# Optimization experiments

Measured on AMD Instinct MI355X. Metric: run time of the kernel, lower is better.

## Reference

```python
import jax, jax.numpy as jnp
import numpy as np

B = 65536   # collocation batch
D = 8       # total_dim (tokens)
H = 128     # subnet hidden_dim
E = 64      # attn_embed_dim == subnet output_dim (proj is None)
NH = 4      # attention heads
GA = 4      # groupA_size


def setup_inputs() -> dict:
    key = jax.random.key(0)
    ks = iter(jax.random.split(key, 32))
    n = lambda shape, s: jax.random.normal(next(ks), shape, dtype=jnp.float32) * s
    inp = {
        "x":  jax.random.normal(next(ks), (B, D), dtype=jnp.float32),
        "w1": n((D, H), 1.0),                 # Lin(1,H) per dim (xavier ~ sqrt(2/(1+H)))
        "b1": jnp.zeros((D, H), jnp.float32),
        "w2": n((D, H, H), 1.0 / np.sqrt(H)),
        "b2": jnp.zeros((D, H), jnp.float32),
        "w3": n((D, E, H), 1.0 / np.sqrt(H)),
        "b3": jnp.zeros((D, E), jnp.float32),
    }
    for tag in ("sa", "sb", "ca", "cb"):
        inp[f"Win_{tag}"] = n((3 * E, E), 1.0 / np.sqrt(E))
        inp[f"bin_{tag}"] = jnp.zeros((3 * E,), jnp.float32)
        inp[f"Wo_{tag}"]  = n((E, E), 1.0 / np.sqrt(E))
        inp[f"bo_{tag}"]  = jnp.zeros((E,), jnp.float32)
    inp["Wf"] = n((1, 2 * E), 1.0 / np.sqrt(2 * E))
    inp["bf"] = jnp.zeros((1,), jnp.float32)
    return inp


def _mha(q, k, v, Win, bin_, Wo, bo):
    # PyTorch nn.MultiheadAttention (batch_first=True) math
    Wq, Wk, Wv = jnp.split(Win, 3, axis=0)
    bq, bk, bv = jnp.split(bin_, 3)
    dh = E // NH
    def heads(t, W, b):
        p = t @ W.T + b                         # [B,S,E]
        return p.reshape(p.shape[0], p.shape[1], NH, dh)
    qh = heads(q, Wq, bq)
    kh = heads(k, Wk, bk)
    vh = heads(v, Wv, bv)
    att = jnp.einsum('bqhd,bkhd->bhqk', qh, kh) / jnp.sqrt(jnp.float32(dh))
    w = jax.nn.softmax(att, axis=-1)
    o = jnp.einsum('bhqk,bkhd->bqhd', w, vh)
    o = o.reshape(o.shape[0], o.shape[1], E)
    return o @ Wo.T + bo


def reference(x, w1, b1, w2, b2, w3, b3,
              Win_sa, bin_sa, Wo_sa, bo_sa,
              Win_sb, bin_sb, Wo_sb, bo_sb,
              Win_ca, bin_ca, Wo_ca, bo_ca,
              Win_cb, bin_cb, Wo_cb, bo_cb,
              Wf, bf):
    # Per-dim subnets as block-diagonal batched matmuls (activation='sin', dropout=0)
    h = jnp.sin(x[:, :, None] * w1[None] + b1[None])            # [B,D,H]
    h = jnp.sin(jnp.einsum('bdh,dkh->bdk', h, w2) + b2[None])   # [B,D,H]
    tokens = jnp.einsum('bdh,doh->bdo', h, w3) + b3[None]       # [B,D,E]

    A = tokens[:, :GA, :]
    Bt = tokens[:, GA:, :]
    A_self  = _mha(A,  A,  A,  Win_sa, bin_sa, Wo_sa, bo_sa)
    B_self  = _mha(Bt, Bt, Bt, Win_sb, bin_sb, Wo_sb, bo_sb)
    A_cross = _mha(A,  Bt, Bt, Win_ca, bin_ca, Wo_ca, bo_ca)
    B_cross = _mha(Bt, A,  A,  Win_cb, bin_cb, Wo_cb, bo_cb)

    A_pool = ((A_self + A_cross) * 0.5).mean(axis=1)            # [B,E]
    B_pool = ((B_self + B_cross) * 0.5).mean(axis=1)            # [B,E]
    combined = jnp.concatenate([A_pool, B_pool], axis=1)        # [B,2E]
    out = combined @ Wf.T + bf                                  # [B,1]
    return jax.nn.leaky_relu(out, 0.01)
```

## Files before the change

kernel.cpp:

```cpp
#include <hip/hip_runtime.h>

typedef unsigned short u16;
typedef __attribute__((ext_vector_type(8))) short short8;
typedef __attribute__((ext_vector_type(4))) float f32x4;

#define OFF_U     0
#define OFF_CV    1024
#define OFF_CONST 1040
#define OFF_CTAG  1044
#define OFF_BA    1056
#define OFF_BB    1328
#define OFF_WA_B    6400
#define OFF_WB_B    41216
#define OFF_W2P_B   76032
#define OFF_W3P_B   338176
#define OFF_TOK_B   469248

#define P_STRIDE 280
#define PSIDE    (32 * P_STRIDE)

static __device__ __forceinline__ u16 f2bf(float f) {
  unsigned int bits = __float_as_uint(f);
  bits += 0x7fffu + ((bits >> 16) & 1u);
  return (u16)(bits >> 16);
}
static __device__ __forceinline__ float bf2f(u16 u) {
  return __uint_as_float(((unsigned int)u) << 16);
}
static __device__ __forceinline__ void ld16(const u16* p, float* o) {
  short8 v0 = *(const short8*)p;
  short8 v1 = *(const short8*)(p + 8);
#pragma unroll
  for (int i = 0; i < 8; i++) {
    o[i] = bf2f((u16)v0[i]);
    o[8 + i] = bf2f((u16)v1[i]);
  }
}

__global__ __launch_bounds__(64) void prep_fold(
    const float* __restrict__ win_sa, const float* __restrict__ bin_sa,
    const float* __restrict__ wo_sa,  const float* __restrict__ bo_sa,
    const float* __restrict__ win_sb, const float* __restrict__ bin_sb,
    const float* __restrict__ wo_sb,  const float* __restrict__ bo_sb,
    const float* __restrict__ win_ca, const float* __restrict__ bin_ca,
    const float* __restrict__ wo_ca,  const float* __restrict__ bo_ca,
    const float* __restrict__ win_cb, const float* __restrict__ bin_cb,
    const float* __restrict__ wo_cb,  const float* __restrict__ bo_cb,
    const float* __restrict__ Wf, float* __restrict__ ws) {
  __shared__ float v_lds[64];
  const int t = threadIdx.x;
  const int tag = blockIdx.x;
  const float* wins[4] = {win_sa, win_sb, win_ca, win_cb};
  const float* bins[4] = {bin_sa, bin_sb, bin_ca, bin_cb};
  const float* wos[4]  = {wo_sa, wo_sb, wo_ca, wo_cb};
  const float* bos[4]  = {bo_sa, bo_sb, bo_ca, bo_cb};
  const float* wfh = Wf + ((tag == 0 || tag == 2) ? 0 : 64);
  float v = 0.f;
#pragma unroll
  for (int e = 0; e < 64; e++) v += wos[tag][e * 64 + t] * wfh[e];
  v_lds[t] = v;
  __syncthreads();
#pragma unroll
  for (int h = 0; h < 4; h++) {
    float u = 0.f;
#pragma unroll
    for (int dp = 0; dp < 16; dp++)
      u += wins[tag][(128 + h * 16 + dp) * 64 + t] * v_lds[h * 16 + dp];
    ws[OFF_U + tag * 256 + h * 64 + t] = u;
  }
  if (t < 4) {
    float cv = 0.f;
#pragma unroll
    for (int dp = 0; dp < 16; dp++)
      cv += bins[tag][128 + t * 16 + dp] * v_lds[t * 16 + dp];
    ws[OFF_CV + tag * 4 + t] = cv;
  }
  if (t == 0) {
    float c = 0.f;
#pragma unroll
    for (int e = 0; e < 64; e++) c += bos[tag][e] * wfh[e];
    ws[OFF_CTAG + tag] = c;
  }
}

__global__ __launch_bounds__(256) void prep_pack(
    const float* __restrict__ w2, const float* __restrict__ w3,
    const float* __restrict__ win_sa, const float* __restrict__ win_sb,
    const float* __restrict__ win_ca, const float* __restrict__ win_cb,
    const float* __restrict__ bin_sa, const float* __restrict__ bin_sb,
    const float* __restrict__ bin_ca, const float* __restrict__ bin_cb,
    const float* __restrict__ bf,
    float* __restrict__ ws, u16* __restrict__ w2p, u16* __restrict__ w3p,
    u16* __restrict__ WA, u16* __restrict__ WB) {
  int idx = blockIdx.x * 256 + threadIdx.x;
  if (idx < 131072) {
    int d = idx >> 14, rem = idx & 16383;
    int f = rem >> 9, ks = f >> 3, nt = f & 7;
    int r2 = rem & 511, l = r2 >> 3, j = r2 & 7;
    int quad = l >> 4, m15 = l & 15;
    w2p[idx] = f2bf(w2[(d * 128 + nt * 16 + m15) * 128 + ks * 32 + quad * 8 + j]);
  } else if (idx < 196608) {
    int i = idx - 131072;
    int d = i >> 13, rem = i & 8191;
    int f = rem >> 9, ks = f >> 2, nt = f & 3;
    int r2 = rem & 511, l = r2 >> 3, j = r2 & 7;
    int quad = l >> 4, m15 = l & 15;
    w3p[i] = f2bf(w3[(d * 64 + nt * 16 + m15) * 128 + ks * 32 + quad * 8 + j]);
  } else if (idx < 214016) {
    int i = idx - 196608;
    int nt = i >> 10, rem = i & 1023;
    int half = rem >> 9, r2 = rem & 511, l = r2 >> 3, j = r2 & 7;
    int n = nt * 16 + (l & 15), k = half * 32 + (l >> 4) * 8 + j;
    float v;
    if (n < 64)       v = win_sa[n * 64 + k] * 0.25f;
    else if (n < 128) v = win_sa[n * 64 + k];
    else if (n < 192) v = win_ca[(n - 128) * 64 + k] * 0.25f;
    else if (n < 256) v = win_cb[(n - 128) * 64 + k];
    else if (n < 260) v = ws[OFF_U + 0 * 256 + (n - 256) * 64 + k];
    else if (n < 264) v = ws[OFF_U + 3 * 256 + (n - 260) * 64 + k];
    else              v = 0.f;
    WA[i] = f2bf(v);
  } else if (idx < 231424) {
    int i = idx - 214016;
    int nt = i >> 10, rem = i & 1023;
    int half = rem >> 9, r2 = rem & 511, l = r2 >> 3, j = r2 & 7;
    int n = nt * 16 + (l & 15), k = half * 32 + (l >> 4) * 8 + j;
    float v;
    if (n < 64)       v = win_sb[n * 64 + k] * 0.25f;
    else if (n < 128) v = win_sb[n * 64 + k];
    else if (n < 192) v = win_cb[(n - 128) * 64 + k] * 0.25f;
    else if (n < 256) v = win_ca[(n - 128) * 64 + k];
    else if (n < 260) v = ws[OFF_U + 1 * 256 + (n - 256) * 64 + k];
    else if (n < 264) v = ws[OFF_U + 2 * 256 + (n - 260) * 64 + k];
    else              v = 0.f;
    WB[i] = f2bf(v);
  } else if (idx < 231696) {
    int n = idx - 231424;
    float v;
    if (n < 64)       v = bin_sa[n] * 0.25f;
    else if (n < 128) v = bin_sa[n];
    else if (n < 192) v = bin_ca[n - 128] * 0.25f;
    else if (n < 256) v = bin_cb[n - 128];
    else if (n < 260) v = ws[OFF_CV + 0 * 4 + (n - 256)];
    else if (n < 264) v = ws[OFF_CV + 3 * 4 + (n - 260)];
    else              v = 0.f;
    ws[OFF_BA + n] = v;
  } else if (idx < 231968) {
    int n = idx - 231696;
    float v;
    if (n < 64)       v = bin_sb[n] * 0.25f;
    else if (n < 128) v = bin_sb[n];
    else if (n < 192) v = bin_cb[n - 128] * 0.25f;
    else if (n < 256) v = bin_ca[n - 128];
    else if (n < 260) v = ws[OFF_CV + 1 * 4 + (n - 256)];
    else if (n < 264) v = ws[OFF_CV + 2 * 4 + (n - 260)];
    else              v = 0.f;
    ws[OFF_BB + n] = v;
  } else if (idx == 231968) {
    ws[OFF_CONST] = 0.5f * (ws[OFF_CTAG] + ws[OFF_CTAG + 1] +
                            ws[OFF_CTAG + 2] + ws[OFF_CTAG + 3]) + bf[0];
  }
}

__global__ __launch_bounds__(256, 3) void tokens_kernel(
    const float* __restrict__ x, const float* __restrict__ w1,
    const float* __restrict__ b1, const float* __restrict__ b2,
    const float* __restrict__ b3, const u16* __restrict__ w2p,
    const u16* __restrict__ w3p, u16* __restrict__ tok_out) {
  __shared__ __align__(16) u16 w2l[16384];
  __shared__ __align__(16) u16 scratch[4][16 * 136];
  const int t = threadIdx.x;
  const int wave = t >> 6, lane = t & 63;
  const int m15 = lane & 15, quad = lane >> 4;
  const int d = blockIdx.x & 7;
  const int g = blockIdx.x >> 3;
  const int b0 = g * 64 + wave * 16;
  const float xv = x[(size_t)(b0 + m15) * 8 + d];
#pragma unroll
  for (int c = 0; c < 8; c++)
    *(short8*)&w2l[c * 2048 + t * 8] = *(const short8*)&w2p[d * 16384 + c * 2048 + t * 8];

  short8 afr[4];
#pragma unroll
  for (int ks = 0; ks < 4; ks++) {
    const float* w1p = w1 + d * 128 + ks * 32 + quad * 8;
    const float* b1p = b1 + d * 128 + ks * 32 + quad * 8;
    float4 wa = *(const float4*)w1p, wb = *(const float4*)(w1p + 4);
    float4 ba = *(const float4*)b1p, bb = *(const float4*)(b1p + 4);
    short8 a;
    a[0] = (short)f2bf(__sinf(xv * wa.x + ba.x));
    a[1] = (short)f2bf(__sinf(xv * wa.y + ba.y));
    a[2] = (short)f2bf(__sinf(xv * wa.z + ba.z));
    a[3] = (short)f2bf(__sinf(xv * wa.w + ba.w));
    a[4] = (short)f2bf(__sinf(xv * wb.x + bb.x));
    a[5] = (short)f2bf(__sinf(xv * wb.y + bb.y));
    a[6] = (short)f2bf(__sinf(xv * wb.z + bb.z));
    a[7] = (short)f2bf(__sinf(xv * wb.w + bb.w));
    afr[ks] = a;
  }
  __syncthreads();
  f32x4 acc2[8];
#pragma unroll
  for (int nt = 0; nt < 8; nt++) acc2[nt] = (f32x4){0.f, 0.f, 0.f, 0.f};
#pragma unroll
  for (int ks = 0; ks < 4; ks++) {
#pragma unroll
    for (int nt = 0; nt < 8; nt++) {
      short8 bfr = *(const short8*)&w2l[(ks * 8 + nt) * 512 + lane * 8];
      acc2[nt] = __builtin_amdgcn_mfma_f32_16x16x32_bf16(afr[ks], bfr, acc2[nt], 0, 0, 0);
    }
  }
#pragma unroll
  for (int nt = 0; nt < 8; nt++) {
    float bias = b2[d * 128 + m15 + 16 * nt];
#pragma unroll
    for (int r = 0; r < 4; r++)
      scratch[wave][(quad * 4 + r) * 136 + m15 + 16 * nt] =
          f2bf(__sinf(acc2[nt][r] + bias));
  }
  const u16* w3base = w3p + d * 8192 + lane * 8;
  f32x4 acc3[4];
#pragma unroll
  for (int nt = 0; nt < 4; nt++) acc3[nt] = (f32x4){0.f, 0.f, 0.f, 0.f};
#pragma unroll
  for (int ks = 0; ks < 4; ks++) {
    short8 af = *(const short8*)(&scratch[wave][m15 * 136 + ks * 32 + quad * 8]);
#pragma unroll
    for (int nt = 0; nt < 4; nt++) {
      short8 bfr = *(const short8*)(w3base + (ks * 4 + nt) * 512);
      acc3[nt] = __builtin_amdgcn_mfma_f32_16x16x32_bf16(af, bfr, acc3[nt], 0, 0, 0);
    }
  }
#pragma unroll
  for (int nt = 0; nt < 4; nt++) {
    float bias = b3[d * 64 + m15 + 16 * nt];
#pragma unroll
    for (int r = 0; r < 4; r++)
      scratch[wave][(quad * 4 + r) * 136 + m15 + 16 * nt] = f2bf(acc3[nt][r] + bias);
  }
  {
    int chunk = lane & 7;
#pragma unroll
    for (int it = 0; it < 2; it++) {
      int row_l = (lane >> 3) + it * 8;
      short8 v = *(const short8*)&scratch[wave][row_l * 136 + chunk * 8];
      *(short8*)(tok_out + ((size_t)(d * 65536 + b0 + row_l)) * 64 + chunk * 8) = v;
    }
  }
}

__global__ __launch_bounds__(128, 4) void attn_kernel(
    const float* __restrict__ ws, const u16* __restrict__ tok,
    const u16* __restrict__ WA, const u16* __restrict__ WB,
    float* __restrict__ out) {
  __shared__ __align__(16) u16 P[2 * PSIDE];
  const int t = threadIdx.x;
  const int wave = t >> 6, lane = t & 63;
  const int m15 = lane & 15, quad = lane >> 4;
  const int side = wave;
  const int b0 = blockIdx.x * 8;
  const float cst = ws[OFF_CONST];

  {
    const u16* W = side ? WB : WA;
    const float* bias = ws + (side ? OFF_BB : OFF_BA);
    const int dd = (m15 & 3) + side * 4;
    short8 a0[2], a1[2];
#pragma unroll
    for (int mt = 0; mt < 2; mt++) {
      const int e = mt * 4 + (m15 >> 2);
      const u16* ab = tok + ((size_t)(dd * 65536 + b0 + e)) * 64 + quad * 8;
      a0[mt] = *(const short8*)ab;
      a1[mt] = *(const short8*)(ab + 32);
    }
    u16* Pb = &P[side * PSIDE];
#pragma unroll
    for (int nt = 0; nt < 17; nt++) {
      const u16* bp = W + nt * 1024 + lane * 8;
      short8 bf0 = *(const short8*)bp;
      short8 bf1 = *(const short8*)(bp + 512);
      float bi = bias[nt * 16 + m15];
#pragma unroll
      for (int mt = 0; mt < 2; mt++) {
        f32x4 acc = {0.f, 0.f, 0.f, 0.f};
        acc = __builtin_amdgcn_mfma_f32_16x16x32_bf16(a0[mt], bf0, acc, 0, 0, 0);
        acc = __builtin_amdgcn_mfma_f32_16x16x32_bf16(a1[mt], bf1, acc, 0, 0, 0);
#pragma unroll
        for (int r = 0; r < 4; r++)
          Pb[(mt * 16 + quad * 4 + r) * P_STRIDE + m15 + 16 * nt] =
              f2bf(acc[r] + bi);
      }
    }
  }
  __syncthreads();
  const int elem = t >> 4, sub = t & 15;
  const int h = sub >> 2, q = sub & 3;
  float acc = 0.f;
#pragma unroll
  for (int tag = 0; tag < 4; tag++) {
    const int qs = tag & 1, cross = tag >> 1;
    const int ks2 = qs ^ cross;
    const u16* Pq = P + qs * PSIDE + (elem * 4 + q) * P_STRIDE + cross * 128 + h * 16;
    float qv[16];
    ld16(Pq, qv);
    const u16* Pk = P + ks2 * PSIDE + (elem * 4) * P_STRIDE + 64 + cross * 128 + h * 16;
    float sc[4];
#pragma unroll
    for (int k = 0; k < 4; k++) {
      float kv[16];
      ld16(Pk + k * P_STRIDE, kv);
      float s = 0.f;
#pragma unroll
      for (int i = 0; i < 16; i++) s += qv[i] * kv[i];
      sc[k] = s;
    }
    float mx = fmaxf(fmaxf(sc[0], sc[1]), fmaxf(sc[2], sc[3]));
    float e0 = __expf(sc[0] - mx), e1 = __expf(sc[1] - mx);
    float e2 = __expf(sc[2] - mx), e3 = __expf(sc[3] - mx);
    const u16* Psv = P + ks2 * PSIDE + (elem * 4) * P_STRIDE + 256 + cross * 4 + h;
    float o = e0 * bf2f(Psv[0]) + e1 * bf2f(Psv[P_STRIDE]) +
              e2 * bf2f(Psv[2 * P_STRIDE]) + e3 * bf2f(Psv[3 * P_STRIDE]);
    acc += o / (e0 + e1 + e2 + e3);
  }
  acc += __shfl_xor(acc, 1);
  acc += __shfl_xor(acc, 2);
  acc += __shfl_xor(acc, 4);
  acc += __shfl_xor(acc, 8);
  if (sub == 0) {
    float val = 0.125f * acc + cst;
    out[b0 + elem] = val > 0.f ? val : 0.01f * val;
  }
}

extern "C" void kernel_launch(void* const* d_in, const int* in_sizes, int n_in,
                              void* d_out, int out_size, void* d_ws, size_t ws_size,
                              hipStream_t stream) {
  const float* x      = (const float*)d_in[0];
  const float* w1     = (const float*)d_in[1];
  const float* b1     = (const float*)d_in[2];
  const float* w2     = (const float*)d_in[3];
  const float* b2     = (const float*)d_in[4];
  const float* w3     = (const float*)d_in[5];
  const float* b3     = (const float*)d_in[6];
  const float* win_sa = (const float*)d_in[7];
  const float* bin_sa = (const float*)d_in[8];
  const float* wo_sa  = (const float*)d_in[9];
  const float* bo_sa  = (const float*)d_in[10];
  const float* win_sb = (const float*)d_in[11];
  const float* bin_sb = (const float*)d_in[12];
  const float* wo_sb  = (const float*)d_in[13];
  const float* bo_sb  = (const float*)d_in[14];
  const float* win_ca = (const float*)d_in[15];
  const float* bin_ca = (const float*)d_in[16];
  const float* wo_ca  = (const float*)d_in[17];
  const float* bo_ca  = (const float*)d_in[18];
  const float* win_cb = (const float*)d_in[19];
  const float* bin_cb = (const float*)d_in[20];
  const float* wo_cb  = (const float*)d_in[21];
  const float* bo_cb  = (const float*)d_in[22];
  const float* Wf     = (const float*)d_in[23];
  const float* bf     = (const float*)d_in[24];
  float* ws = (float*)d_ws;
  u16* WAp    = (u16*)((char*)d_ws + OFF_WA_B);
  u16* WBp    = (u16*)((char*)d_ws + OFF_WB_B);
  u16* w2p    = (u16*)((char*)d_ws + OFF_W2P_B);
  u16* w3p    = (u16*)((char*)d_ws + OFF_W3P_B);
  u16* tokbuf = (u16*)((char*)d_ws + OFF_TOK_B);
  float* out = (float*)d_out;

  prep_fold<<<4, 64, 0, stream>>>(win_sa, bin_sa, wo_sa, bo_sa,
                                  win_sb, bin_sb, wo_sb, bo_sb,
                                  win_ca, bin_ca, wo_ca, bo_ca,
                                  win_cb, bin_cb, wo_cb, bo_cb,
                                  Wf, ws);
  prep_pack<<<907, 256, 0, stream>>>(w2, w3, win_sa, win_sb, win_ca, win_cb,
                                     bin_sa, bin_sb, bin_ca, bin_cb, bf,
                                     ws, w2p, w3p, WAp, WBp);
  tokens_kernel<<<8192, 256, 0, stream>>>(x, w1, b1, b2, b3, w2p, w3p, tokbuf);
  attn_kernel<<<8192, 128, 0, stream>>>(ws, tokbuf, WAp, WBp, out);
}
```

Before: 227.9 us.

## Use MFMA for attention scores, pack transposed P stores, drop W2 LDS staging

The attention scoring stage now computes the per-head QK dot products with a bf16 MFMA over a transposed P layout instead of scalar loops. The softmax also drops max subtraction and uses a fast reciprocal. The projection MFMA swaps its operands so each lane writes four packed bf16 values in one 8-byte store. The tokens kernel reads W2 fragments straight from global memory instead of staging them in LDS, which removes a sync and frees LDS for a higher occupancy bound (4 blocks). Risks: exp overflow without max subtraction, the MFMA computes redundant off-diagonal products, and global W2 reads depend on cache hits.

```diff
diff --git a/kernel.cpp b/kernel.cpp
--- a/kernel.cpp
+++ b/kernel.cpp
@@ -2,7 +2,9 @@
 
 typedef unsigned short u16;
 typedef __attribute__((ext_vector_type(8))) short short8;
+typedef __attribute__((ext_vector_type(4))) short s16x4;
 typedef __attribute__((ext_vector_type(4))) float f32x4;
+typedef __attribute__((ext_vector_type(2))) unsigned int u32x2;
 
 #define OFF_U     0
 #define OFF_CV    1024
@@ -24,17 +26,12 @@
   bits += 0x7fffu + ((bits >> 16) & 1u);
   return (u16)(bits >> 16);
 }
+static __device__ __forceinline__ unsigned rbits(float f) {
+  unsigned b = __float_as_uint(f);
+  return b + 0x7fffu + ((b >> 16) & 1u);
+}
 static __device__ __forceinline__ float bf2f(u16 u) {
   return __uint_as_float(((unsigned int)u) << 16);
-}
-static __device__ __forceinline__ void ld16(const u16* p, float* o) {
-  short8 v0 = *(const short8*)p;
-  short8 v1 = *(const short8*)(p + 8);
-#pragma unroll
-  for (int i = 0; i < 8; i++) {
-    o[i] = bf2f((u16)v0[i]);
-    o[8 + i] = bf2f((u16)v1[i]);
-  }
 }
 
 __global__ __launch_bounds__(64) void prep_fold(
@@ -162,12 +159,11 @@
   }
 }
 
-__global__ __launch_bounds__(256, 3) void tokens_kernel(
+__global__ __launch_bounds__(256, 4) void tokens_kernel(
     const float* __restrict__ x, const float* __restrict__ w1,
     const float* __restrict__ b1, const float* __restrict__ b2,
     const float* __restrict__ b3, const u16* __restrict__ w2p,
     const u16* __restrict__ w3p, u16* __restrict__ tok_out) {
-  __shared__ __align__(16) u16 w2l[16384];
   __shared__ __align__(16) u16 scratch[4][16 * 136];
   const int t = threadIdx.x;
   const int wave = t >> 6, lane = t & 63;
@@ -176,9 +172,6 @@
   const int g = blockIdx.x >> 3;
   const int b0 = g * 64 + wave * 16;
   const float xv = x[(size_t)(b0 + m15) * 8 + d];
-#pragma unroll
-  for (int c = 0; c < 8; c++)
-    *(short8*)&w2l[c * 2048 + t * 8] = *(const short8*)&w2p[d * 16384 + c * 2048 + t * 8];
 
   short8 afr[4];
 #pragma unroll
@@ -198,7 +191,7 @@
     a[7] = (short)f2bf(__sinf(xv * wb.w + bb.w));
     afr[ks] = a;
   }
-  __syncthreads();
+  const u16* w2base = w2p + d * 16384 + lane * 8;
   f32x4 acc2[8];
 #pragma unroll
   for (int nt = 0; nt < 8; nt++) acc2[nt] = (f32x4){0.f, 0.f, 0.f, 0.f};
@@ -206,7 +199,7 @@
   for (int ks = 0; ks < 4; ks++) {
 #pragma unroll
     for (int nt = 0; nt < 8; nt++) {
-      short8 bfr = *(const short8*)&w2l[(ks * 8 + nt) * 512 + lane * 8];
+      short8 bfr = *(const short8*)(w2base + (ks * 8 + nt) * 512);
       acc2[nt] = __builtin_amdgcn_mfma_f32_16x16x32_bf16(afr[ks], bfr, acc2[nt], 0, 0, 0);
     }
   }
@@ -277,58 +270,62 @@
 #pragma unroll
     for (int nt = 0; nt < 17; nt++) {
       const u16* bp = W + nt * 1024 + lane * 8;
-      short8 bf0 = *(const short8*)bp;
-      short8 bf1 = *(const short8*)(bp + 512);
-      float bi = bias[nt * 16 + m15];
+      short8 w0f = *(const short8*)bp;
+      short8 w1f = *(const short8*)(bp + 512);
+      float4 bi = *(const float4*)(bias + nt * 16 + quad * 4);
 #pragma unroll
       for (int mt = 0; mt < 2; mt++) {
         f32x4 acc = {0.f, 0.f, 0.f, 0.f};
-        acc = __builtin_amdgcn_mfma_f32_16x16x32_bf16(a0[mt], bf0, acc, 0, 0, 0);
-        acc = __builtin_amdgcn_mfma_f32_16x16x32_bf16(a1[mt], bf1, acc, 0, 0, 0);
-#pragma unroll
-        for (int r = 0; r < 4; r++)
-          Pb[(mt * 16 + quad * 4 + r) * P_STRIDE + m15 + 16 * nt] =
-              f2bf(acc[r] + bi);
+        acc = __builtin_amdgcn_mfma_f32_16x16x32_bf16(w0f, a0[mt], acc, 0, 0, 0);
+        acc = __builtin_amdgcn_mfma_f32_16x16x32_bf16(w1f, a1[mt], acc, 0, 0, 0);
+        u32x2 pk;
+        pk[0] = (rbits(acc[1] + bi.y) & 0xffff0000u) | (rbits(acc[0] + bi.x) >> 16);
+        pk[1] = (rbits(acc[3] + bi.w) & 0xffff0000u) | (rbits(acc[2] + bi.z) >> 16);
+        *(u32x2*)&Pb[(mt * 16 + m15) * P_STRIDE + nt * 16 + quad * 4] = pk;
       }
     }
   }
   __syncthreads();
-  const int elem = t >> 4, sub = t & 15;
-  const int h = sub >> 2, q = sub & 3;
-  float acc = 0.f;
-#pragma unroll
-  for (int tag = 0; tag < 4; tag++) {
-    const int qs = tag & 1, cross = tag >> 1;
-    const int ks2 = qs ^ cross;
-    const u16* Pq = P + qs * PSIDE + (elem * 4 + q) * P_STRIDE + cross * 128 + h * 16;
-    float qv[16];
-    ld16(Pq, qv);
-    const u16* Pk = P + ks2 * PSIDE + (elem * 4) * P_STRIDE + 64 + cross * 128 + h * 16;
-    float sc[4];
-#pragma unroll
-    for (int k = 0; k < 4; k++) {
-      float kv[16];
-      ld16(Pk + k * P_STRIDE, kv);
-      float s = 0.f;
-#pragma unroll
-      for (int i = 0; i < 16; i++) s += qv[i] * kv[i];
-      sc[k] = s;
-    }
-    float mx = fmaxf(fmaxf(sc[0], sc[1]), fmaxf(sc[2], sc[3]));
-    float e0 = __expf(sc[0] - mx), e1 = __expf(sc[1] - mx);
-    float e2 = __expf(sc[2] - mx), e3 = __expf(sc[3] - mx);
-    const u16* Psv = P + ks2 * PSIDE + (elem * 4) * P_STRIDE + 256 + cross * 4 + h;
-    float o = e0 * bf2f(Psv[0]) + e1 * bf2f(Psv[P_STRIDE]) +
-              e2 * bf2f(Psv[2 * P_STRIDE]) + e3 * bf2f(Psv[3 * P_STRIDE]);
-    acc += o / (e0 + e1 + e2 + e3);
-  }
-  acc += __shfl_xor(acc, 1);
-  acc += __shfl_xor(acc, 2);
-  acc += __shfl_xor(acc, 4);
-  acc += __shfl_xor(acc, 8);
-  if (sub == 0) {
-    float val = 0.125f * acc + cst;
-    out[b0 + elem] = val > 0.f ? val : 0.01f * val;
+  {
+    const int eg = wave;
+    const int q2 = (quad & 1) * 8;
+    const bool hiq = (quad & 2) != 0;
+    const u16* row0 = P + (size_t)(eg * 16 + m15) * P_STRIDE;
+    const u16* row1 = row0 + PSIDE;
+    float acc = 0.f;
+#pragma unroll
+    for (int tag = 0; tag < 4; tag++) {
+      const int qs = tag & 1, cross = tag >> 1;
+      const int ks2 = qs ^ cross;
+      const u16* rowK = ks2 ? row1 : row0;
+      const u16* rowQ = qs ? row1 : row0;
+      const u16* vbase = P + ks2 * PSIDE +
+                         (size_t)(eg * 16 + quad * 4) * P_STRIDE + 256 + cross * 4;
+      s16x4 vv0 = *(const s16x4*)(vbase);
+      s16x4 vv1 = *(const s16x4*)(vbase + P_STRIDE);
+      s16x4 vv2 = *(const s16x4*)(vbase + 2 * P_STRIDE);
+      s16x4 vv3 = *(const s16x4*)(vbase + 3 * P_STRIDE);
+#pragma unroll
+      for (int h = 0; h < 4; h++) {
+        const int kcol = 64 + cross * 128 + h * 16 + q2;
+        const int qcol = hiq ? 264 : (cross * 128 + h * 16 + q2);
+        short8 afr = *(const short8*)(rowK + kcol);
+        short8 bfr = *(const short8*)(rowQ + qcol);
+        f32x4 c = {0.f, 0.f, 0.f, 0.f};
+        c = __builtin_amdgcn_mfma_f32_16x16x32_bf16(afr, bfr, c, 0, 0, 0);
+        float e0 = __expf(c[0]), e1 = __expf(c[1]);
+        float e2 = __expf(c[2]), e3 = __expf(c[3]);
+        float o = e0 * bf2f((u16)vv0[h]) + e1 * bf2f((u16)vv1[h]) +
+                  e2 * bf2f((u16)vv2[h]) + e3 * bf2f((u16)vv3[h]);
+        acc += o * __builtin_amdgcn_rcpf(e0 + e1 + e2 + e3);
+      }
+    }
+    acc += __shfl_xor(acc, 1);
+    acc += __shfl_xor(acc, 2);
+    if (quad == (m15 >> 2) && (m15 & 3) == 0) {
+      float val = 0.125f * acc + cst;
+      out[b0 + eg * 4 + quad] = val > 0.f ? val : 0.01f * val;
+    }
   }
 }
 
```

Result: no change. 229.0 us (+0.5%).
